# Performance work log

Measured on AMD Instinct MI355X. Metric: run time of the kernel, lower is better.

## Reference

```python
import jax, jax.numpy as jnp
import numpy as np
import math

STEPSIZE = 0.1
ALPHA = 20.0      # note: the alpha constraint-correction term is computed but DISCARDED in the
                  # original (`grad_final` is built but `grad` is returned) -- we replicate that.
M_CLIP = 1000.0
N, D = 64, 32


def _proj(x):
    g = 2.0 * x
    s = jnp.sum(g * g)
    return jnp.eye(x.shape[0], dtype=x.dtype) - jnp.outer(g, g) / s


def _step(particle, mu):
    n, d = particle.shape
    x = particle
    # log-prob grad for logp_i = -0.5||x_i - mu||^2  ->  s_j = mu - x_j
    s_grad = mu - x                                       # (n, d)
    # pairwise squared distances; bandwidth h uses numpy-style median, detached (as in torch)
    diff = x[:, None, :] - x[None, :, :]
    dist2 = jnp.sum(diff * diff, axis=-1)                 # (n, n)
    h = jax.lax.stop_gradient(jnp.median(dist2)) / math.log(n)
    denom = h + 1e-6
    Kmat = jnp.exp(-dist2 / denom)                        # (n, n) rbf kernel
    Dmat = jax.vmap(_proj)(x)                             # (n, d, d) projection matrices

    # mle term: grad_i += sum_j D_i (k_ij I) D_j s_j  =  D_i @ (Kmat @ (D_j s_j))
    Ds = jnp.einsum('jab,jb->ja', Dmat, s_grad)           # (n, d)
    mle = jnp.einsum('iab,ij,jb->ia', Dmat, Kmat, Ds)     # (n, d)

    # repulsion/derivative term: t_ij[k1] = sum_k2 d K_ij[k1,k2] / d x_j[k2]
    # where K_ij = D(x_i) * k(x_i, x_j) * D(x_j). When i == j the same variable appears in
    # both slots (torch autograd accumulates both), handled via the `same` flag + where.
    def K_pair(xj, xi_c, same):
        xi = jnp.where(same, xj, xi_c)
        k = jnp.exp(-jnp.sum((xi - xj) ** 2) / denom)
        return _proj(xi) @ (k * _proj(xj))                # (d, d)

    def pair_term(xi_c, xj, same):
        J = jax.jacfwd(K_pair)(xj, xi_c, same)            # (d, d, d)
        return jnp.einsum('abb->a', J)                    # (d,)

    ii, jj = jnp.meshgrid(jnp.arange(n), jnp.arange(n), indexing='ij')
    same = (ii == jj).reshape(-1)
    xi_all = x[ii.reshape(-1)]
    xj_all = x[jj.reshape(-1)]
    T = jax.vmap(pair_term)(xi_all, xj_all, same).reshape(n, n, d)
    deriv = jnp.sum(T, axis=1)                            # (n, d)

    grad = (mle + deriv) / n                              # alpha term dropped, as in source
    dx = jnp.clip(grad * STEPSIZE, -M_CLIP, M_CLIP)
    return particle + dx


def setup_inputs() -> dict:
    key = jax.random.key(0)
    k1, k2 = jax.random.split(key)
    particle = jax.random.normal(k1, (N, D), dtype=jnp.float32)
    mu = jax.random.normal(k2, (D,), dtype=jnp.float32)
    return {"particle": particle, "mu": mu}


def reference(particle, mu):
    return _step(particle, mu)
```

## Files before the change

kernel.cpp:

```cpp
#include <hip/hip_runtime.h>
#include <math.h>

#define NP 64
#define DD 32
#define NTHREADS 1024
#define NB 8
#define NBUK 4096

__device__ __forceinline__ float readlane_f(float v, int lane) {
    return __int_as_float(__builtin_amdgcn_readlane(__float_as_int(v), lane));
}

__global__ __launch_bounds__(NTHREADS)
void svgd_kernel(const float* __restrict__ particle,
                 const float* __restrict__ mu,
                 float* __restrict__ out) {
    __shared__ float    sNarr[NP];
    __shared__ float4   jinfo[NP];
    __shared__ float    dist2[NP*NP];
    __shared__ uint2    wmm[16];
    __shared__ unsigned hist[NBUK];
    __shared__ unsigned resv[2];
    __shared__ float4   wpart[3*64];
    __shared__ float    kpart[3*64];
    __shared__ float    invdS;

    const int tid  = threadIdx.x;
    const int lane = tid & 63;
    const int wv   = tid >> 6;
    const int i0   = blockIdx.x * 8;

    #pragma unroll
    for (int k = 0; k < NBUK/NTHREADS; ++k) hist[tid + k*NTHREADS] = 0u;

    float4 xq[8];
    #pragma unroll
    for (int k = 0; k < 8; ++k) xq[k] = ((const float4*)particle)[lane*8 + k];
    float xv[DD];
    #pragma unroll
    for (int k = 0; k < 8; ++k) {
        xv[4*k+0] = xq[k].x; xv[4*k+1] = xq[k].y;
        xv[4*k+2] = xq[k].z; xv[4*k+3] = xq[k].w;
    }
    float sj = 0.f;
    #pragma unroll
    for (int d = 0; d < DD; ++d) sj = fmaf(xv[d], xv[d], sj);

    if (wv == 0) {
        sNarr[lane] = sj;
        float mreg = mu[lane & 31];
        float mdot = 0.f;
        #pragma unroll
        for (int d = 0; d < DD; ++d) mdot = fmaf(readlane_f(mreg, d), xv[d], mdot);
        float inv_sj = 1.0f / sj;
        jinfo[lane] = make_float4(sj, inv_sj, -mdot*inv_sj, 0.f);
    }

    unsigned ubr[4];
    unsigned tmn = 0xFFFFFFFFu, tmx = 0u;
    #pragma unroll
    for (int r = 0; r < 4; ++r) {
        int i = wv*4 + r;
        float acc = 0.f;
        #pragma unroll
        for (int d = 0; d < DD; ++d) acc = fmaf(readlane_f(xv[d], i), xv[d], acc);
        float si = readlane_f(sj, i);
        float d2 = si + sj - 2.f*acc;
        dist2[i*64 + lane] = d2;
        unsigned ub = __float_as_uint(d2);
        ubr[r] = ub;
        if (i < lane) {
            tmn = ub < tmn ? ub : tmn;
            tmx = ub > tmx ? ub : tmx;
        }
    }
    #pragma unroll
    for (int m = 32; m >= 1; m >>= 1) {
        unsigned on = (unsigned)__shfl_xor((int)tmn, m, 64);
        unsigned ox = (unsigned)__shfl_xor((int)tmx, m, 64);
        tmn = on < tmn ? on : tmn;
        tmx = ox > tmx ? ox : tmx;
    }
    if (lane == 0) wmm[wv] = make_uint2(tmn, tmx);
    __syncthreads();

    unsigned mnv = 0xFFFFFFFFu, mx = 0u;
    #pragma unroll
    for (int k = 0; k < 16; ++k) {
        uint2 wm = wmm[k];
        mnv = wm.x < mnv ? wm.x : mnv;
        mx  = wm.y > mx  ? wm.y : mx;
    }
    int shift = 15;
    unsigned range = (mx >> shift) - (mnv >> shift);
    while (range > (unsigned)(NBUK-1)) {
        ++shift;
        range = (mx >> shift) - (mnv >> shift);
    }
    const unsigned base = mnv >> shift;
    #pragma unroll
    for (int r = 0; r < 4; ++r) {
        int i = wv*4 + r;
        if (i < lane) atomicAdd(&hist[(ubr[r] >> shift) - base], 1u);
    }
    __syncthreads();

    if (wv == 0) {
        int nb = (int)range + 1;
        int chunk = (nb + 63) >> 6;
        int st = lane * chunk;
        unsigned tot = 0;
        for (int c = 0; c < chunk; ++c) {
            int b = st + c;
            if (b < nb) tot += hist[b];
        }
        unsigned inc = tot;
        #pragma unroll
        for (int m = 1; m < 64; m <<= 1) {
            unsigned o = (unsigned)__shfl_up((int)inc, m, 64);
            if (lane >= m) inc += o;
        }
        unsigned excl = inc - tot;
        #pragma unroll
        for (int rk = 0; rk < 2; ++rk) {
            unsigned target = 991u + (unsigned)rk;
            if (excl <= target && target < excl + tot) {
                unsigned cum = excl; int b = st;
                for (;;) {
                    unsigned c = hist[b];
                    if (cum + c > target) break;
                    cum += c; ++b;
                }
                resv[rk] = (base + (unsigned)b) << shift;
            }
        }
        __builtin_amdgcn_s_waitcnt(0);
        if (lane == 0) {
            float med = 0.5f*(__uint_as_float(resv[0]) + __uint_as_float(resv[1]));
            float denom = med * (1.0f/4.1588830833596715f) + 1e-6f;
            invdS = 1.0f / denom;
        }
    }
    __syncthreads();

    {
        const float invd = invdS;
        float4 w4 = make_float4(0.f,0.f,0.f,0.f);
        float  kacc = 0.f;
        if (tid < 256) {
            int h  = tid >> 6;
            int il = (tid >> 3) & 7;
            int q  = tid & 7;
            int i  = i0 + il;
            float si = sNarr[i];
            float4 xr[16];
            #pragma unroll
            for (int jj = 0; jj < 16; ++jj)
                xr[jj] = ((const float4*)particle)[(h*16 + jj)*8 + q];
            #pragma unroll
            for (int jj = 0; jj < 16; ++jj) {
                int j = h*16 + jj;
                float4 ji = jinfo[j];
                float d2  = dist2[j*64 + i];
                float K   = __expf(-d2 * invd);
                float u   = d2 - si - ji.x;
                float t1  = fmaf(invd, u, -(float)(DD-1));
                float E   = K * fmaf(t1, ji.y, ji.z);
                float4 x4 = xr[jj];
                w4.x = fmaf(E, x4.x, w4.x);
                w4.y = fmaf(E, x4.y, w4.y);
                w4.z = fmaf(E, x4.z, w4.z);
                w4.w = fmaf(E, x4.w, w4.w);
                kacc += K;
            }
            if (h > 0) {
                wpart[(h-1)*64 + (tid & 63)] = w4;
                kpart[(h-1)*64 + (tid & 63)] = kacc;
            }
        }
        __syncthreads();
        if (tid < 64) {
            #pragma unroll
            for (int p = 0; p < 3; ++p) {
                float4 wp = wpart[p*64 + tid];
                w4.x += wp.x; w4.y += wp.y; w4.z += wp.z; w4.w += wp.w;
                kacc += kpart[p*64 + tid];
            }
            int il = tid >> 3, q = tid & 7;
            int i  = i0 + il;
            float4 xi4 = ((const float4*)particle)[i*8 + q];
            float4 mu4 = ((const float4*)mu)[q];
            float4 ji  = jinfo[i];
            float  c2  = 2.f*invd*kacc;
            w4.x += kacc*mu4.x + c2*xi4.x;
            w4.y += kacc*mu4.y + c2*xi4.y;
            w4.z += kacc*mu4.z + c2*xi4.z;
            w4.w += kacc*mu4.w + c2*xi4.w;
            float rdot = xi4.x*w4.x + xi4.y*w4.y + xi4.z*w4.z + xi4.w*w4.w;
            rdot += __shfl_xor(rdot, 1, 64);
            rdot += __shfl_xor(rdot, 2, 64);
            rdot += __shfl_xor(rdot, 4, 64);
            float s3 = (rdot + (float)(DD-1)) * ji.y;
            float gx = (w4.x - xi4.x*s3) * (1.f/(float)NP);
            float gy = (w4.y - xi4.y*s3) * (1.f/(float)NP);
            float gz = (w4.z - xi4.z*s3) * (1.f/(float)NP);
            float gw = (w4.w - xi4.w*s3) * (1.f/(float)NP);
            float4 o4;
            o4.x = xi4.x + fminf(fmaxf(0.1f*gx, -1000.f), 1000.f);
            o4.y = xi4.y + fminf(fmaxf(0.1f*gy, -1000.f), 1000.f);
            o4.z = xi4.z + fminf(fmaxf(0.1f*gz, -1000.f), 1000.f);
            o4.w = xi4.w + fminf(fmaxf(0.1f*gw, -1000.f), 1000.f);
            ((float4*)out)[i*8 + q] = o4;
        }
    }
}

extern "C" void kernel_launch(void* const* d_in, const int* in_sizes, int n_in,
                              void* d_out, int out_size, void* d_ws, size_t ws_size,
                              hipStream_t stream) {
    const float* particle = (const float*)d_in[0];
    const float* mu       = (const float*)d_in[1];
    float* outp           = (float*)d_out;
    hipLaunchKernelGGL(svgd_kernel, dim3(NB), dim3(NTHREADS), 0, stream,
                       particle, mu, outp);
}
```

Measured before the change: 14.10 us.

## Redundant per-wave median select and shuffle-reduced row accumulation, fewer barriers

```diff
diff --git a/kernel.cpp b/kernel.cpp
--- a/kernel.cpp
+++ b/kernel.cpp
@@ -5,7 +5,8 @@
 #define DD 32
 #define NTHREADS 1024
 #define NB 8
-#define NBUK 4096
+#define NBUK 1024
+#define HSZ (NBUK + NBUK/16)
 
 __device__ __forceinline__ float readlane_f(float v, int lane) {
     return __int_as_float(__builtin_amdgcn_readlane(__float_as_int(v), lane));
@@ -19,19 +20,15 @@
     __shared__ float4   jinfo[NP];
     __shared__ float    dist2[NP*NP];
     __shared__ uint2    wmm[16];
-    __shared__ unsigned hist[NBUK];
-    __shared__ unsigned resv[2];
-    __shared__ float4   wpart[3*64];
-    __shared__ float    kpart[3*64];
-    __shared__ float    invdS;
+    __shared__ unsigned hist[HSZ];
 
     const int tid  = threadIdx.x;
     const int lane = tid & 63;
     const int wv   = tid >> 6;
     const int i0   = blockIdx.x * 8;
 
-    #pragma unroll
-    for (int k = 0; k < NBUK/NTHREADS; ++k) hist[tid + k*NTHREADS] = 0u;
+    hist[tid] = 0u;
+    if (tid < HSZ - NBUK) hist[NBUK + tid] = 0u;
 
     float4 xq[8];
     #pragma unroll
@@ -101,118 +98,109 @@
     #pragma unroll
     for (int r = 0; r < 4; ++r) {
         int i = wv*4 + r;
-        if (i < lane) atomicAdd(&hist[(ubr[r] >> shift) - base], 1u);
+        if (i < lane) {
+            unsigned b = (ubr[r] >> shift) - base;
+            atomicAdd(&hist[b + (b >> 4)], 1u);
+        }
+    }
+
+    const int jg = lane >> 3;
+    const int q  = lane & 7;
+    float4 xr[8], xi4, mu4;
+    if (wv < 8) {
+        #pragma unroll
+        for (int jj = 0; jj < 8; ++jj)
+            xr[jj] = ((const float4*)particle)[(jj*8 + jg)*8 + q];
+        xi4 = ((const float4*)particle)[(i0 + wv)*8 + q];
+        mu4 = ((const float4*)mu)[q];
     }
     __syncthreads();
 
-    if (wv == 0) {
-        int nb = (int)range + 1;
-        int chunk = (nb + 63) >> 6;
-        int st = lane * chunk;
-        unsigned tot = 0;
-        for (int c = 0; c < chunk; ++c) {
-            int b = st + c;
-            if (b < nb) tot += hist[b];
+    if (wv >= 8) return;
+
+    unsigned creg[16];
+    #pragma unroll
+    for (int c = 0; c < 16; ++c) creg[c] = hist[17*lane + c];
+    unsigned tot = 0;
+    #pragma unroll
+    for (int c = 0; c < 16; ++c) tot += creg[c];
+    unsigned inc = tot;
+    #pragma unroll
+    for (int m = 1; m < 64; m <<= 1) {
+        unsigned o = (unsigned)__shfl_up((int)inc, m, 64);
+        if (lane >= m) inc += o;
+    }
+    const unsigned excl = inc - tot;
+
+    unsigned vbits[2];
+    #pragma unroll
+    for (int rk = 0; rk < 2; ++rk) {
+        unsigned target = 991u + (unsigned)rk;
+        bool cond = (excl <= target) && (target < inc);
+        unsigned long long mask = __ballot(cond);
+        int owner = (int)(__ffsll((long long)mask) - 1);
+        unsigned cum = excl; int bl = 0; bool done = false;
+        #pragma unroll
+        for (int c = 0; c < 16; ++c) {
+            cum += creg[c];
+            if (!done && cum > target) { bl = c; done = true; }
         }
-        unsigned inc = tot;
-        #pragma unroll
-        for (int m = 1; m < 64; m <<= 1) {
-            unsigned o = (unsigned)__shfl_up((int)inc, m, 64);
-            if (lane >= m) inc += o;
-        }
-        unsigned excl = inc - tot;
-        #pragma unroll
-        for (int rk = 0; rk < 2; ++rk) {
-            unsigned target = 991u + (unsigned)rk;
-            if (excl <= target && target < excl + tot) {
-                unsigned cum = excl; int b = st;
-                for (;;) {
-                    unsigned c = hist[b];
-                    if (cum + c > target) break;
-                    cum += c; ++b;
-                }
-                resv[rk] = (base + (unsigned)b) << shift;
-            }
-        }
-        __builtin_amdgcn_s_waitcnt(0);
-        if (lane == 0) {
-            float med = 0.5f*(__uint_as_float(resv[0]) + __uint_as_float(resv[1]));
-            float denom = med * (1.0f/4.1588830833596715f) + 1e-6f;
-            invdS = 1.0f / denom;
-        }
-    }
-    __syncthreads();
-
-    {
-        const float invd = invdS;
-        float4 w4 = make_float4(0.f,0.f,0.f,0.f);
-        float  kacc = 0.f;
-        if (tid < 256) {
-            int h  = tid >> 6;
-            int il = (tid >> 3) & 7;
-            int q  = tid & 7;
-            int i  = i0 + il;
-            float si = sNarr[i];
-            float4 xr[16];
-            #pragma unroll
-            for (int jj = 0; jj < 16; ++jj)
-                xr[jj] = ((const float4*)particle)[(h*16 + jj)*8 + q];
-            #pragma unroll
-            for (int jj = 0; jj < 16; ++jj) {
-                int j = h*16 + jj;
-                float4 ji = jinfo[j];
-                float d2  = dist2[j*64 + i];
-                float K   = __expf(-d2 * invd);
-                float u   = d2 - si - ji.x;
-                float t1  = fmaf(invd, u, -(float)(DD-1));
-                float E   = K * fmaf(t1, ji.y, ji.z);
-                float4 x4 = xr[jj];
-                w4.x = fmaf(E, x4.x, w4.x);
-                w4.y = fmaf(E, x4.y, w4.y);
-                w4.z = fmaf(E, x4.z, w4.z);
-                w4.w = fmaf(E, x4.w, w4.w);
-                kacc += K;
-            }
-            if (h > 0) {
-                wpart[(h-1)*64 + (tid & 63)] = w4;
-                kpart[(h-1)*64 + (tid & 63)] = kacc;
-            }
-        }
-        __syncthreads();
-        if (tid < 64) {
-            #pragma unroll
-            for (int p = 0; p < 3; ++p) {
-                float4 wp = wpart[p*64 + tid];
-                w4.x += wp.x; w4.y += wp.y; w4.z += wp.z; w4.w += wp.w;
-                kacc += kpart[p*64 + tid];
-            }
-            int il = tid >> 3, q = tid & 7;
-            int i  = i0 + il;
-            float4 xi4 = ((const float4*)particle)[i*8 + q];
-            float4 mu4 = ((const float4*)mu)[q];
-            float4 ji  = jinfo[i];
-            float  c2  = 2.f*invd*kacc;
-            w4.x += kacc*mu4.x + c2*xi4.x;
-            w4.y += kacc*mu4.y + c2*xi4.y;
-            w4.z += kacc*mu4.z + c2*xi4.z;
-            w4.w += kacc*mu4.w + c2*xi4.w;
-            float rdot = xi4.x*w4.x + xi4.y*w4.y + xi4.z*w4.z + xi4.w*w4.w;
-            rdot += __shfl_xor(rdot, 1, 64);
-            rdot += __shfl_xor(rdot, 2, 64);
-            rdot += __shfl_xor(rdot, 4, 64);
-            float s3 = (rdot + (float)(DD-1)) * ji.y;
-            float gx = (w4.x - xi4.x*s3) * (1.f/(float)NP);
-            float gy = (w4.y - xi4.y*s3) * (1.f/(float)NP);
-            float gz = (w4.z - xi4.z*s3) * (1.f/(float)NP);
-            float gw = (w4.w - xi4.w*s3) * (1.f/(float)NP);
-            float4 o4;
-            o4.x = xi4.x + fminf(fmaxf(0.1f*gx, -1000.f), 1000.f);
-            o4.y = xi4.y + fminf(fmaxf(0.1f*gy, -1000.f), 1000.f);
-            o4.z = xi4.z + fminf(fmaxf(0.1f*gz, -1000.f), 1000.f);
-            o4.w = xi4.w + fminf(fmaxf(0.1f*gw, -1000.f), 1000.f);
-            ((float4*)out)[i*8 + q] = o4;
-        }
-    }
+        int bucket = lane*16 + bl;
+        int bsel = __shfl(bucket, owner, 64);
+        vbits[rk] = (base + (unsigned)bsel) << shift;
+    }
+    float med   = 0.5f*(__uint_as_float(vbits[0]) + __uint_as_float(vbits[1]));
+    float denom = med * (1.0f/4.1588830833596715f) + 1e-6f;
+    const float invd = 1.0f / denom;
+
+    const int i = i0 + wv;
+    const float si = sNarr[i];
+    float4 w4 = make_float4(0.f,0.f,0.f,0.f);
+    float  kacc = 0.f;
+    #pragma unroll
+    for (int jj = 0; jj < 8; ++jj) {
+        int j = jj*8 + jg;
+        float4 ji = jinfo[j];
+        float d2  = dist2[i*64 + j];
+        float K   = __expf(-d2 * invd);
+        float u   = d2 - si - ji.x;
+        float E   = K * fmaf(fmaf(invd, u, -(float)(DD-1)), ji.y, ji.z);
+        float4 x4 = xr[jj];
+        w4.x = fmaf(E, x4.x, w4.x);
+        w4.y = fmaf(E, x4.y, w4.y);
+        w4.z = fmaf(E, x4.z, w4.z);
+        w4.w = fmaf(E, x4.w, w4.w);
+        kacc += K;
+    }
+    #pragma unroll
+    for (int m = 8; m <= 32; m <<= 1) {
+        w4.x += __shfl_xor(w4.x, m, 64);
+        w4.y += __shfl_xor(w4.y, m, 64);
+        w4.z += __shfl_xor(w4.z, m, 64);
+        w4.w += __shfl_xor(w4.w, m, 64);
+        kacc += __shfl_xor(kacc, m, 64);
+    }
+    float4 ji_i = jinfo[i];
+    float  c2   = 2.f*invd*kacc;
+    w4.x += kacc*mu4.x + c2*xi4.x;
+    w4.y += kacc*mu4.y + c2*xi4.y;
+    w4.z += kacc*mu4.z + c2*xi4.z;
+    w4.w += kacc*mu4.w + c2*xi4.w;
+    float rdot = xi4.x*w4.x + xi4.y*w4.y + xi4.z*w4.z + xi4.w*w4.w;
+    rdot += __shfl_xor(rdot, 1, 64);
+    rdot += __shfl_xor(rdot, 2, 64);
+    rdot += __shfl_xor(rdot, 4, 64);
+    float s3 = (rdot + (float)(DD-1)) * ji_i.y;
+    float gx = (w4.x - xi4.x*s3) * (1.f/(float)NP);
+    float gy = (w4.y - xi4.y*s3) * (1.f/(float)NP);
+    float gz = (w4.z - xi4.z*s3) * (1.f/(float)NP);
+    float gw = (w4.w - xi4.w*s3) * (1.f/(float)NP);
+    float4 o4;
+    o4.x = xi4.x + fminf(fmaxf(0.1f*gx, -1000.f), 1000.f);
+    o4.y = xi4.y + fminf(fmaxf(0.1f*gy, -1000.f), 1000.f);
+    o4.z = xi4.z + fminf(fmaxf(0.1f*gz, -1000.f), 1000.f);
+    o4.w = xi4.w + fminf(fmaxf(0.1f*gw, -1000.f), 1000.f);
+    if (lane < 8) ((float4*)out)[i*8 + q] = o4;
 }
 
 extern "C" void kernel_launch(void* const* d_in, const int* in_sizes, int n_in,
```

Result: no change. 14.29 us (+1.4%).
